# Optimization experiments

Measured on AMD Instinct MI355X. Metric: run time of the kernel, lower is better.

The kernel has to match this reference:

```python
import jax, jax.numpy as jnp
import numpy as np

N_COMPONENTS = 16
N_FEATURES = 64
N_SAMPLES = 200000


def setup_inputs() -> dict:
    key = jax.random.key(0)
    k_data, k_means, k_cov = jax.random.split(key, 3)
    data = jax.random.normal(k_data, (N_SAMPLES, N_FEATURES), dtype=jnp.float32)
    weights = jnp.ones((N_COMPONENTS,), dtype=jnp.float32) / N_COMPONENTS
    means = jax.random.normal(k_means, (N_COMPONENTS, N_FEATURES), dtype=jnp.float32)
    # SPD covariances: A A^T / d + I (module inits to identity; use realistic SPD here)
    A = jax.random.normal(k_cov, (N_COMPONENTS, N_FEATURES, N_FEATURES), dtype=jnp.float32)
    covariances = jnp.einsum('kij,klj->kil', A, A) / N_FEATURES + jnp.eye(N_FEATURES, dtype=jnp.float32)
    return {"data": data, "weights": weights, "means": means, "covariances": covariances}


def reference(data, weights, means, covariances):
    # data: [N, d]; weights: [K]; means: [K, d]; covariances: [K, d, d]
    d = data.shape[1]
    L = jnp.linalg.cholesky(covariances)                      # [K, d, d]
    diff = data[None, :, :] - means[:, None, :]               # [K, N, d]
    # Solve L y = diff^T per component (batched triangular solve)
    y = jax.scipy.linalg.solve_triangular(L, jnp.swapaxes(diff, -1, -2), lower=True)  # [K, d, N]
    maha = jnp.sum(y * y, axis=1)                             # [K, N]
    half_logdet = jnp.sum(jnp.log(jnp.diagonal(L, axis1=-2, axis2=-1)), axis=-1)      # [K]
    log2pi = jnp.log(jnp.array(2.0 * np.pi, dtype=data.dtype))
    log_probs = -0.5 * (maha + d * log2pi) - half_logdet[:, None]                     # [K, N]
    weighted_log_probs = log_probs + jnp.log(weights)[:, None]
    log_sum_exp = jax.scipy.special.logsumexp(weighted_log_probs, axis=0)             # [N]
    return jnp.sum(log_sum_exp)
```

## Files before the change

### kernel.cpp

```cpp
#include <hip/hip_runtime.h>
#include <hip/hip_bf16.h>
#include <math.h>

#define NF 64
#define NC 16
#define MAIN_BLOCKS 256
#define MAIN_WAVES  13
#define TPW 4

typedef __bf16 bf16x8 __attribute__((ext_vector_type(8)));
typedef float f32x4 __attribute__((ext_vector_type(4)));
typedef unsigned int u32;

__device__ __forceinline__ void stage16(const void* gsrc, void* ldst) {
    __builtin_amdgcn_global_load_lds(
        (const __attribute__((address_space(1))) u32*)gsrc,
        (__attribute__((address_space(3))) u32*)ldst,
        16, 0, 0);
}

__global__ __launch_bounds__(256) void gmm_precompute(
    const float* __restrict__ cov,
    const float* __restrict__ means,
    const float* __restrict__ weights,
    __hip_bfloat16* __restrict__ g,
    float* __restrict__ t,
    float* __restrict__ Cc)
{
    const int w = threadIdx.x >> 6;
    const int c = threadIdx.x & 63;
    const int k = blockIdx.x;

    __shared__ __align__(16) float LT[NF][68];
    __shared__ float Xs[NF][65];
    __shared__ __align__(16) float wb2[2][68];
    __shared__ __align__(16) float gw2[2][68];

    float a_loc[16];
    {
        const float* src = cov + (long)k * NF * NF + (w * 16) * NF + c;
        #pragma unroll
        for (int r = 0; r < 16; ++r)
            a_loc[r] = src[r * NF];
    }

    float rsq_loc[16];
    float logdiag = 0.0f;

    #pragma unroll 1
    for (int q = 0; q < 4; ++q) {
        #pragma unroll
        for (int jj = 0; jj < 16; ++jj) {
            float* wb = wb2[jj & 1];
            if (w == q) wb[c] = a_loc[jj];
            __syncthreads();
            const int j = q * 16 + jj;
            float ajc = wb[c];
            float d   = wb[j];
            float sq  = sqrtf(d);
            float rsq = __builtin_amdgcn_rcpf(sq);
            float rd  = __builtin_amdgcn_rcpf(d);
            logdiag += 0.5f * __logf(d);
            if (w == q) rsq_loc[jj] = rsq;
            LT[j][c] = ajc * rsq;
            float beta = ajc * rd;
            const float4* wv = (const float4*)(wb + w * 16);
            #pragma unroll
            for (int rr = 0; rr < 16; rr += 4) {
                float4 v = wv[rr >> 2];
                a_loc[rr]     = fmaf(-v.x, beta, a_loc[rr]);
                a_loc[rr + 1] = fmaf(-v.y, beta, a_loc[rr + 1]);
                a_loc[rr + 2] = fmaf(-v.z, beta, a_loc[rr + 2]);
                a_loc[rr + 3] = fmaf(-v.w, beta, a_loc[rr + 3]);
            }
        }
    }

    float s_loc[16];
    #pragma unroll
    for (int r = 0; r < 16; ++r)
        s_loc[r] = (w * 16 + r == c) ? 1.0f : 0.0f;

    #pragma unroll 1
    for (int q = 0; q < 4; ++q) {
        #pragma unroll
        for (int ii = 0; ii < 16; ++ii) {
            const int i = q * 16 + ii;
            float* gw = gw2[ii & 1];
            if (w == q) {
                float gv = s_loc[ii] * rsq_loc[ii];
                gw[c] = gv;
                Xs[i][c] = gv;
            }
            __syncthreads();
            float gc = gw[c];
            const float4* lv4 = (const float4*)(&LT[i][w * 16]);
            #pragma unroll
            for (int rr = 0; rr < 16; rr += 4) {
                float4 v = lv4[rr >> 2];
                s_loc[rr]     = fmaf(-v.x, gc, s_loc[rr]);
                s_loc[rr + 1] = fmaf(-v.y, gc, s_loc[rr + 1]);
                s_loc[rr + 2] = fmaf(-v.z, gc, s_loc[rr + 2]);
                s_loc[rr + 3] = fmaf(-v.w, gc, s_loc[rr + 3]);
            }
        }
    }
    __syncthreads();

    {
        __hip_bfloat16* grow = g + ((long)(k * NF + c)) * NF;
        #pragma unroll
        for (int h = 0; h < 2; ++h) {
            int jb = w * 2 + h;
            bf16x8 v;
            #pragma unroll
            for (int u = 0; u < 8; ++u)
                v[u] = (__bf16)Xs[c][jb * 8 + u];
            *(bf16x8*)(grow + ((jb ^ (c & 7)) * 8)) = v;
        }
    }

    if (w == 0) {
        const float* mu = means + k * NF;
        float a0 = 0.0f, a1 = 0.0f;
        #pragma unroll
        for (int j = 0; j < NF; j += 2) {
            a0 = fmaf(Xs[c][j],     mu[j],     a0);
            a1 = fmaf(Xs[c][j + 1], mu[j + 1], a1);
        }
        t[k * NF + c] = a0 + a1;
        if (c == 0)
            Cc[k] = __logf(weights[k]) - 0.5f * (float)NF * 1.8378770664093453f - logdiag;
    }
}

__global__ __launch_bounds__(832) void gmm_main(
    const float* __restrict__ data,
    const char* __restrict__ gsw,
    const float* __restrict__ t,
    const float* __restrict__ Cc,
    float* __restrict__ partials,
    int nTiles, int N, int totalWaves)
{
    __shared__ __align__(16) char gbuf[NC * 8192];
    __shared__ __align__(16) float nt_lds[NC * NF];
    __shared__ float cc_lds[NC];

    const int tidx = threadIdx.x;
    const int w    = tidx >> 6;
    const int lane = tidx & 63;
    const int l15  = lane & 15;
    const int lg   = lane >> 4;

    for (int i = w; i < NC; i += MAIN_WAVES) {
        const char* src = gsw + (size_t)i * 8192;
        char* dst = gbuf + (size_t)i * 8192;
        #pragma unroll
        for (int u = 0; u < 8; ++u)
            stage16(src + u * 1024 + lane * 16, dst + u * 1024);
    }

    for (int i = tidx; i < NC * NF; i += 64 * MAIN_WAVES) nt_lds[i] = -t[i];
    if (tidx < NC) cc_lds[tidx] = Cc[tidx];

    const int gid = blockIdx.x * MAIN_WAVES + w;

    int offA[4], offB[4];
    #pragma unroll
    for (int rc = 0; rc < 4; ++rc) {
        int row = rc * 16 + l15;
        offA[rc] = row * 128 + ((lg       ^ (l15 & 7)) * 16);
        offB[rc] = row * 128 + (((lg + 4) ^ (l15 & 7)) * 16);
    }

    bf16x8 xf[TPW][2];
    if (gid < nTiles) {
        const long base = (long)gid * (TPW * 16);
        #pragma unroll
        for (int st = 0; st < TPW; ++st) {
            long row = base + st * 16 + l15;
            if (row > (long)N - 1) row = (long)N - 1;
            const float* xp = data + row * NF + lg * 8;
            float4 a0 = *(const float4*)(xp);
            float4 a1 = *(const float4*)(xp + 4);
            float4 b0 = *(const float4*)(xp + 32);
            float4 b1 = *(const float4*)(xp + 36);
            bf16x8 f0, f1;
            f0[0] = (__bf16)a0.x; f0[1] = (__bf16)a0.y;
            f0[2] = (__bf16)a0.z; f0[3] = (__bf16)a0.w;
            f0[4] = (__bf16)a1.x; f0[5] = (__bf16)a1.y;
            f0[6] = (__bf16)a1.z; f0[7] = (__bf16)a1.w;
            f1[0] = (__bf16)b0.x; f1[1] = (__bf16)b0.y;
            f1[2] = (__bf16)b0.z; f1[3] = (__bf16)b0.w;
            f1[4] = (__bf16)b1.x; f1[5] = (__bf16)b1.y;
            f1[6] = (__bf16)b1.z; f1[7] = (__bf16)b1.w;
            xf[st][0] = f0;
            xf[st][1] = f1;
        }
    }

    __syncthreads();

    float wavePartial = 0.0f;

    #pragma unroll 1
    for (int tile = gid; tile < nTiles; tile += totalWaves) {
        const long base = (long)tile * (TPW * 16);
        if (tile != gid) {
            #pragma unroll
            for (int st = 0; st < TPW; ++st) {
                long row = base + st * 16 + l15;
                if (row > (long)N - 1) row = (long)N - 1;
                const float* xp = data + row * NF + lg * 8;
                float4 a0 = *(const float4*)(xp);
                float4 a1 = *(const float4*)(xp + 4);
                float4 b0 = *(const float4*)(xp + 32);
                float4 b1 = *(const float4*)(xp + 36);
                bf16x8 f0, f1;
                f0[0] = (__bf16)a0.x; f0[1] = (__bf16)a0.y;
                f0[2] = (__bf16)a0.z; f0[3] = (__bf16)a0.w;
                f0[4] = (__bf16)a1.x; f0[5] = (__bf16)a1.y;
                f0[6] = (__bf16)a1.z; f0[7] = (__bf16)a1.w;
                f1[0] = (__bf16)b0.x; f1[1] = (__bf16)b0.y;
                f1[2] = (__bf16)b0.z; f1[3] = (__bf16)b0.w;
                f1[4] = (__bf16)b1.x; f1[5] = (__bf16)b1.y;
                f1[6] = (__bf16)b1.z; f1[7] = (__bf16)b1.w;
                xf[st][0] = f0;
                xf[st][1] = f1;
            }
        }

        float m[TPW], s[TPW];
        #pragma unroll
        for (int st = 0; st < TPW; ++st) { m[st] = -INFINITY; s[st] = 0.0f; }

        #pragma unroll 2
        for (int ii = 0; ii < NC; ++ii) {
            const int kk = (ii + w) & (NC - 1);
            float mah[TPW];
            #pragma unroll
            for (int st = 0; st < TPW; ++st) mah[st] = 0.0f;

            const char* gk = gbuf + kk * 8192;
            const float* ntk = &nt_lds[kk * NF];

            #pragma unroll
            for (int rc = 0; rc < 2; ++rc) {
                bf16x8 ga = *(const bf16x8*)(gk + offA[rc]);
                f32x4 ntv = *(const f32x4*)(ntk + rc * 16 + lg * 4);
                #pragma unroll
                for (int st = 0; st < TPW; ++st) {
                    f32x4 acc = ntv;
                    acc = __builtin_amdgcn_mfma_f32_16x16x32_bf16(ga, xf[st][0], acc, 0, 0, 0);
                    mah[st] = fmaf(acc[0], acc[0], mah[st]);
                    mah[st] = fmaf(acc[1], acc[1], mah[st]);
                    mah[st] = fmaf(acc[2], acc[2], mah[st]);
                    mah[st] = fmaf(acc[3], acc[3], mah[st]);
                }
            }
            #pragma unroll
            for (int rc = 2; rc < 4; ++rc) {
                bf16x8 ga = *(const bf16x8*)(gk + offA[rc]);
                bf16x8 gb = *(const bf16x8*)(gk + offB[rc]);
                f32x4 ntv = *(const f32x4*)(ntk + rc * 16 + lg * 4);
                #pragma unroll
                for (int st = 0; st < TPW; ++st) {
                    f32x4 acc = ntv;
                    acc = __builtin_amdgcn_mfma_f32_16x16x32_bf16(ga, xf[st][0], acc, 0, 0, 0);
                    acc = __builtin_amdgcn_mfma_f32_16x16x32_bf16(gb, xf[st][1], acc, 0, 0, 0);
                    mah[st] = fmaf(acc[0], acc[0], mah[st]);
                    mah[st] = fmaf(acc[1], acc[1], mah[st]);
                    mah[st] = fmaf(acc[2], acc[2], mah[st]);
                    mah[st] = fmaf(acc[3], acc[3], mah[st]);
                }
            }

            float Ck = cc_lds[kk];
            float wlp[TPW];
            float dmax = -INFINITY;
            #pragma unroll
            for (int st = 0; st < TPW; ++st) {
                float v = mah[st];
                v += __shfl_xor(v, 16);
                v += __shfl_xor(v, 32);
                wlp[st] = fmaf(-0.5f, v, Ck);
                dmax = fmaxf(dmax, wlp[st] - m[st]);
            }
            if (__any(dmax > 60.0f)) {
                #pragma unroll
                for (int st = 0; st < TPW; ++st) {
                    float mn = fmaxf(m[st], wlp[st]);
                    s[st] = s[st] * __expf(m[st] - mn) + __expf(wlp[st] - mn);
                    m[st] = mn;
                }
            } else {
                #pragma unroll
                for (int st = 0; st < TPW; ++st)
                    s[st] += __expf(wlp[st] - m[st]);
            }
        }

        if (lg == 0) {
            #pragma unroll
            for (int st = 0; st < TPW; ++st) {
                long sid = base + st * 16 + l15;
                if (sid < (long)N)
                    wavePartial += m[st] + __logf(s[st]);
            }
        }
    }

    #pragma unroll
    for (int off = 1; off < 64; off <<= 1)
        wavePartial += __shfl_xor(wavePartial, off);
    if (lane == 0)
        partials[gid] = wavePartial;
}

__global__ __launch_bounds__(256) void gmm_reduce(
    const float* __restrict__ partials, int n, float* __restrict__ out)
{
    float s = 0.0f;
    for (int i = threadIdx.x; i < n; i += 256)
        s += partials[i];
    #pragma unroll
    for (int off = 1; off < 64; off <<= 1)
        s += __shfl_xor(s, off);
    __shared__ float sm[4];
    const int wave = threadIdx.x >> 6;
    const int lane = threadIdx.x & 63;
    if (lane == 0) sm[wave] = s;
    __syncthreads();
    if (threadIdx.x == 0)
        out[0] = (sm[0] + sm[1]) + (sm[2] + sm[3]);
}

extern "C" void kernel_launch(void* const* d_in, const int* in_sizes, int n_in,
                              void* d_out, int out_size, void* d_ws, size_t ws_size,
                              hipStream_t stream)
{
    const float* data    = (const float*)d_in[0];
    const float* weights = (const float*)d_in[1];
    const float* means   = (const float*)d_in[2];
    const float* cov     = (const float*)d_in[3];

    const int N = in_sizes[0] / NF;

    char* ws = (char*)d_ws;
    __hip_bfloat16* g = (__hip_bfloat16*)ws;
    float* t          = (float*)(ws + 131072);
    float* Cc         = (float*)(ws + 131072 + 4096);
    float* partials   = (float*)(ws + 131072 + 4096 + 64);

    const int nTiles     = (N + TPW * 16 - 1) / (TPW * 16);
    const int totalWaves = MAIN_BLOCKS * MAIN_WAVES;

    gmm_precompute<<<NC, 256, 0, stream>>>(cov, means, weights, g, t, Cc);
    gmm_main<<<MAIN_BLOCKS, 64 * MAIN_WAVES, 0, stream>>>(
        data, (const char*)g, t, Cc, partials, nTiles, N, totalWaves);
    gmm_reduce<<<1, 256, 0, stream>>>(partials, totalWaves, (float*)d_out);
}
```

Before: 65.04 us.

## Fuse Cholesky precompute into main kernel with global flag barrier

Merges the per-component Cholesky/inverse precompute into the main GMM kernel. The first 16 blocks do the factorization while the other blocks prefetch their data tiles, then every block spins on a global atomic counter before staging the factors into LDS. The aim is to remove a kernel launch boundary and overlap the data loads with the serial precompute. In exchange it adds a memset, a spin-wait that assumes all 256 blocks are co-resident, and a slower precompute that now runs inside a large 832-thread block.

```diff
diff --git a/kernel.cpp b/kernel.cpp
--- a/kernel.cpp
+++ b/kernel.cpp
@@ -19,163 +19,40 @@
         16, 0, 0);
 }
 
-__global__ __launch_bounds__(256) void gmm_precompute(
+__global__ __launch_bounds__(832) void gmm_fused(
     const float* __restrict__ cov,
     const float* __restrict__ means,
     const float* __restrict__ weights,
+    const float* __restrict__ data,
     __hip_bfloat16* __restrict__ g,
     float* __restrict__ t,
-    float* __restrict__ Cc)
-{
-    const int w = threadIdx.x >> 6;
-    const int c = threadIdx.x & 63;
-    const int k = blockIdx.x;
-
-    __shared__ __align__(16) float LT[NF][68];
-    __shared__ float Xs[NF][65];
-    __shared__ __align__(16) float wb2[2][68];
-    __shared__ __align__(16) float gw2[2][68];
-
-    float a_loc[16];
-    {
-        const float* src = cov + (long)k * NF * NF + (w * 16) * NF + c;
-        #pragma unroll
-        for (int r = 0; r < 16; ++r)
-            a_loc[r] = src[r * NF];
-    }
-
-    float rsq_loc[16];
-    float logdiag = 0.0f;
-
-    #pragma unroll 1
-    for (int q = 0; q < 4; ++q) {
-        #pragma unroll
-        for (int jj = 0; jj < 16; ++jj) {
-            float* wb = wb2[jj & 1];
-            if (w == q) wb[c] = a_loc[jj];
-            __syncthreads();
-            const int j = q * 16 + jj;
-            float ajc = wb[c];
-            float d   = wb[j];
-            float sq  = sqrtf(d);
-            float rsq = __builtin_amdgcn_rcpf(sq);
-            float rd  = __builtin_amdgcn_rcpf(d);
-            logdiag += 0.5f * __logf(d);
-            if (w == q) rsq_loc[jj] = rsq;
-            LT[j][c] = ajc * rsq;
-            float beta = ajc * rd;
-            const float4* wv = (const float4*)(wb + w * 16);
-            #pragma unroll
-            for (int rr = 0; rr < 16; rr += 4) {
-                float4 v = wv[rr >> 2];
-                a_loc[rr]     = fmaf(-v.x, beta, a_loc[rr]);
-                a_loc[rr + 1] = fmaf(-v.y, beta, a_loc[rr + 1]);
-                a_loc[rr + 2] = fmaf(-v.z, beta, a_loc[rr + 2]);
-                a_loc[rr + 3] = fmaf(-v.w, beta, a_loc[rr + 3]);
-            }
-        }
-    }
-
-    float s_loc[16];
-    #pragma unroll
-    for (int r = 0; r < 16; ++r)
-        s_loc[r] = (w * 16 + r == c) ? 1.0f : 0.0f;
-
-    #pragma unroll 1
-    for (int q = 0; q < 4; ++q) {
-        #pragma unroll
-        for (int ii = 0; ii < 16; ++ii) {
-            const int i = q * 16 + ii;
-            float* gw = gw2[ii & 1];
-            if (w == q) {
-                float gv = s_loc[ii] * rsq_loc[ii];
-                gw[c] = gv;
-                Xs[i][c] = gv;
-            }
-            __syncthreads();
-            float gc = gw[c];
-            const float4* lv4 = (const float4*)(&LT[i][w * 16]);
-            #pragma unroll
-            for (int rr = 0; rr < 16; rr += 4) {
-                float4 v = lv4[rr >> 2];
-                s_loc[rr]     = fmaf(-v.x, gc, s_loc[rr]);
-                s_loc[rr + 1] = fmaf(-v.y, gc, s_loc[rr + 1]);
-                s_loc[rr + 2] = fmaf(-v.z, gc, s_loc[rr + 2]);
-                s_loc[rr + 3] = fmaf(-v.w, gc, s_loc[rr + 3]);
-            }
-        }
-    }
-    __syncthreads();
-
-    {
-        __hip_bfloat16* grow = g + ((long)(k * NF + c)) * NF;
-        #pragma unroll
-        for (int h = 0; h < 2; ++h) {
-            int jb = w * 2 + h;
-            bf16x8 v;
-            #pragma unroll
-            for (int u = 0; u < 8; ++u)
-                v[u] = (__bf16)Xs[c][jb * 8 + u];
-            *(bf16x8*)(grow + ((jb ^ (c & 7)) * 8)) = v;
-        }
-    }
-
-    if (w == 0) {
-        const float* mu = means + k * NF;
-        float a0 = 0.0f, a1 = 0.0f;
-        #pragma unroll
-        for (int j = 0; j < NF; j += 2) {
-            a0 = fmaf(Xs[c][j],     mu[j],     a0);
-            a1 = fmaf(Xs[c][j + 1], mu[j + 1], a1);
-        }
-        t[k * NF + c] = a0 + a1;
-        if (c == 0)
-            Cc[k] = __logf(weights[k]) - 0.5f * (float)NF * 1.8378770664093453f - logdiag;
-    }
-}
-
-__global__ __launch_bounds__(832) void gmm_main(
-    const float* __restrict__ data,
-    const char* __restrict__ gsw,
-    const float* __restrict__ t,
-    const float* __restrict__ Cc,
+    float* __restrict__ Cc,
+    unsigned int* __restrict__ flag,
     float* __restrict__ partials,
     int nTiles, int N, int totalWaves)
 {
-    __shared__ __align__(16) char gbuf[NC * 8192];
-    __shared__ __align__(16) float nt_lds[NC * NF];
-    __shared__ float cc_lds[NC];
-
+    __shared__ __align__(16) char smem[135232];
+    char*  gbuf   = smem;
+    float* nt_lds = (float*)(smem + 131072);
+    float* cc_lds = (float*)(smem + 131072 + 4096);
+    float* LTb  = (float*)smem;
+    float* Xsb  = (float*)(smem + 17408);
+    float* wb2b = (float*)(smem + 34048);
+    float* gw2b = (float*)(smem + 34592);
+
+    const int bid  = blockIdx.x;
     const int tidx = threadIdx.x;
     const int w    = tidx >> 6;
     const int lane = tidx & 63;
     const int l15  = lane & 15;
     const int lg   = lane >> 4;
-
-    for (int i = w; i < NC; i += MAIN_WAVES) {
-        const char* src = gsw + (size_t)i * 8192;
-        char* dst = gbuf + (size_t)i * 8192;
-        #pragma unroll
-        for (int u = 0; u < 8; ++u)
-            stage16(src + u * 1024 + lane * 16, dst + u * 1024);
-    }
-
-    for (int i = tidx; i < NC * NF; i += 64 * MAIN_WAVES) nt_lds[i] = -t[i];
-    if (tidx < NC) cc_lds[tidx] = Cc[tidx];
-
-    const int gid = blockIdx.x * MAIN_WAVES + w;
-
-    int offA[4], offB[4];
-    #pragma unroll
-    for (int rc = 0; rc < 4; ++rc) {
-        int row = rc * 16 + l15;
-        offA[rc] = row * 128 + ((lg       ^ (l15 & 7)) * 16);
-        offB[rc] = row * 128 + (((lg + 4) ^ (l15 & 7)) * 16);
-    }
+    const bool isPre = (bid < NC);
+
+    const int gid = bid * MAIN_WAVES + w;
+    const bool haveTile = (gid < nTiles);
 
     bf16x8 xf[TPW][2];
-    if (gid < nTiles) {
-        const long base = (long)gid * (TPW * 16);
+    auto loadx = [&](long base) {
         #pragma unroll
         for (int st = 0; st < TPW; ++st) {
             long row = base + st * 16 + l15;
@@ -197,6 +74,147 @@
             xf[st][0] = f0;
             xf[st][1] = f1;
         }
+    };
+
+    if (!isPre && haveTile)
+        loadx((long)gid * (TPW * 16));
+
+    if (isPre) {
+        const int k = bid;
+        const int c = lane;
+
+        float a_loc[16], rsq_loc[16];
+        float logdiag = 0.0f;
+        if (w < 4) {
+            const float* src = cov + (long)k * NF * NF + (w * 16) * NF + c;
+            #pragma unroll
+            for (int r = 0; r < 16; ++r)
+                a_loc[r] = src[r * NF];
+        }
+
+        #pragma unroll 1
+        for (int q = 0; q < 4; ++q) {
+            #pragma unroll
+            for (int jj = 0; jj < 16; ++jj) {
+                float* wb = wb2b + (jj & 1) * 68;
+                if (w == q) wb[c] = a_loc[jj];
+                __syncthreads();
+                const int j = q * 16 + jj;
+                if (w < 4) {
+                    float ajc = wb[c];
+                    float d   = wb[j];
+                    float sq  = sqrtf(d);
+                    float rsq = __builtin_amdgcn_rcpf(sq);
+                    float rd  = __builtin_amdgcn_rcpf(d);
+                    logdiag += 0.5f * __logf(d);
+                    if (w == q) rsq_loc[jj] = rsq;
+                    if (w == 0) LTb[j * 68 + c] = ajc * rsq;
+                    float beta = ajc * rd;
+                    const float4* wv = (const float4*)(wb + w * 16);
+                    #pragma unroll
+                    for (int rr = 0; rr < 16; rr += 4) {
+                        float4 v = wv[rr >> 2];
+                        a_loc[rr]     = fmaf(-v.x, beta, a_loc[rr]);
+                        a_loc[rr + 1] = fmaf(-v.y, beta, a_loc[rr + 1]);
+                        a_loc[rr + 2] = fmaf(-v.z, beta, a_loc[rr + 2]);
+                        a_loc[rr + 3] = fmaf(-v.w, beta, a_loc[rr + 3]);
+                    }
+                }
+            }
+        }
+
+        float s_loc[16];
+        if (w < 4) {
+            #pragma unroll
+            for (int r = 0; r < 16; ++r)
+                s_loc[r] = (w * 16 + r == c) ? 1.0f : 0.0f;
+        }
+        #pragma unroll 1
+        for (int q = 0; q < 4; ++q) {
+            #pragma unroll
+            for (int ii = 0; ii < 16; ++ii) {
+                const int i = q * 16 + ii;
+                float* gw = gw2b + (ii & 1) * 68;
+                if (w == q) {
+                    float gv = s_loc[ii] * rsq_loc[ii];
+                    gw[c] = gv;
+                    Xsb[i * 65 + c] = gv;
+                }
+                __syncthreads();
+                if (w < 4) {
+                    float gc = gw[c];
+                    const float4* lv4 = (const float4*)(LTb + i * 68 + w * 16);
+                    #pragma unroll
+                    for (int rr = 0; rr < 16; rr += 4) {
+                        float4 v = lv4[rr >> 2];
+                        s_loc[rr]     = fmaf(-v.x, gc, s_loc[rr]);
+                        s_loc[rr + 1] = fmaf(-v.y, gc, s_loc[rr + 1]);
+                        s_loc[rr + 2] = fmaf(-v.z, gc, s_loc[rr + 2]);
+                        s_loc[rr + 3] = fmaf(-v.w, gc, s_loc[rr + 3]);
+                    }
+                }
+            }
+        }
+        __syncthreads();
+
+        if (w < 4) {
+            __hip_bfloat16* grow = g + ((long)(k * NF + c)) * NF;
+            #pragma unroll
+            for (int h = 0; h < 2; ++h) {
+                int jb = w * 2 + h;
+                bf16x8 v;
+                #pragma unroll
+                for (int u = 0; u < 8; ++u)
+                    v[u] = (__bf16)Xsb[c * 65 + jb * 8 + u];
+                *(bf16x8*)(grow + ((jb ^ (c & 7)) * 8)) = v;
+            }
+        }
+        if (w == 0) {
+            const float* mu = means + k * NF;
+            float a0 = 0.0f, a1 = 0.0f;
+            #pragma unroll
+            for (int j = 0; j < NF; j += 2) {
+                a0 = fmaf(Xsb[j * 65 + c],       mu[j],     a0);
+                a1 = fmaf(Xsb[(j + 1) * 65 + c], mu[j + 1], a1);
+            }
+            t[k * NF + c] = a0 + a1;
+            if (c == 0)
+                Cc[k] = __logf(weights[k]) - 0.5f * (float)NF * 1.8378770664093453f - logdiag;
+        }
+        __syncthreads();
+        if (tidx == 0) {
+            __threadfence();
+            atomicAdd(flag, 1u);
+        }
+    }
+
+    if (tidx == 0) {
+        volatile unsigned int* vf = (volatile unsigned int*)flag;
+        while (*vf < (unsigned int)NC)
+            __builtin_amdgcn_s_sleep(2);
+    }
+    __syncthreads();
+    __threadfence();
+
+    for (int i = w; i < NC; i += MAIN_WAVES) {
+        const char* src = (const char*)g + (size_t)i * 8192;
+        char* dst = gbuf + (size_t)i * 8192;
+        #pragma unroll
+        for (int u = 0; u < 8; ++u)
+            stage16(src + u * 1024 + lane * 16, dst + u * 1024);
+    }
+    for (int i = tidx; i < NC * NF; i += 64 * MAIN_WAVES) nt_lds[i] = -t[i];
+    if (tidx < NC) cc_lds[tidx] = Cc[tidx];
+
+    if (isPre && haveTile)
+        loadx((long)gid * (TPW * 16));
+
+    int offA[4], offB[4];
+    #pragma unroll
+    for (int rc = 0; rc < 4; ++rc) {
+        int row = rc * 16 + l15;
+        offA[rc] = row * 128 + ((lg       ^ (l15 & 7)) * 16);
+        offB[rc] = row * 128 + (((lg + 4) ^ (l15 & 7)) * 16);
     }
 
     __syncthreads();
@@ -206,29 +224,7 @@
     #pragma unroll 1
     for (int tile = gid; tile < nTiles; tile += totalWaves) {
         const long base = (long)tile * (TPW * 16);
-        if (tile != gid) {
-            #pragma unroll
-            for (int st = 0; st < TPW; ++st) {
-                long row = base + st * 16 + l15;
-                if (row > (long)N - 1) row = (long)N - 1;
-                const float* xp = data + row * NF + lg * 8;
-                float4 a0 = *(const float4*)(xp);
-                float4 a1 = *(const float4*)(xp + 4);
-                float4 b0 = *(const float4*)(xp + 32);
-                float4 b1 = *(const float4*)(xp + 36);
-                bf16x8 f0, f1;
-                f0[0] = (__bf16)a0.x; f0[1] = (__bf16)a0.y;
-                f0[2] = (__bf16)a0.z; f0[3] = (__bf16)a0.w;
-                f0[4] = (__bf16)a1.x; f0[5] = (__bf16)a1.y;
-                f0[6] = (__bf16)a1.z; f0[7] = (__bf16)a1.w;
-                f1[0] = (__bf16)b0.x; f1[1] = (__bf16)b0.y;
-                f1[2] = (__bf16)b0.z; f1[3] = (__bf16)b0.w;
-                f1[4] = (__bf16)b1.x; f1[5] = (__bf16)b1.y;
-                f1[6] = (__bf16)b1.z; f1[7] = (__bf16)b1.w;
-                xf[st][0] = f0;
-                xf[st][1] = f1;
-            }
-        }
+        if (tile != gid) loadx(base);
 
         float m[TPW], s[TPW];
         #pragma unroll
@@ -347,16 +343,18 @@
     const int N = in_sizes[0] / NF;
 
     char* ws = (char*)d_ws;
-    __hip_bfloat16* g = (__hip_bfloat16*)ws;
-    float* t          = (float*)(ws + 131072);
-    float* Cc         = (float*)(ws + 131072 + 4096);
-    float* partials   = (float*)(ws + 131072 + 4096 + 64);
+    __hip_bfloat16* g   = (__hip_bfloat16*)ws;
+    float* t            = (float*)(ws + 131072);
+    float* Cc           = (float*)(ws + 131072 + 4096);
+    unsigned int* flag  = (unsigned int*)(ws + 131072 + 4096 + 64);
+    float* partials     = (float*)(ws + 131072 + 4096 + 64 + 64);
 
     const int nTiles     = (N + TPW * 16 - 1) / (TPW * 16);
     const int totalWaves = MAIN_BLOCKS * MAIN_WAVES;
 
-    gmm_precompute<<<NC, 256, 0, stream>>>(cov, means, weights, g, t, Cc);
-    gmm_main<<<MAIN_BLOCKS, 64 * MAIN_WAVES, 0, stream>>>(
-        data, (const char*)g, t, Cc, partials, nTiles, N, totalWaves);
+    hipMemsetAsync(flag, 0, sizeof(unsigned int), stream);
+
+    gmm_fused<<<MAIN_BLOCKS, 64 * MAIN_WAVES, 0, stream>>>(
+        cov, means, weights, data, g, t, Cc, flag, partials, nTiles, N, totalWaves);
     gmm_reduce<<<1, 256, 0, stream>>>(partials, totalWaves, (float*)d_out);
 }
```

Result: slower. 122.4 us (+88.1%).
